# Kernel optimization log

Hardware: AMD Instinct MI355X
Metric: run time of the kernel (lower is better)

## Reference

```python
import jax, jax.numpy as jnp
import numpy as np

N_NODES = 50000


def _gcn_norm(edge_index, num_nodes):
    # Add self-loops (PyG GCNConv default) and compute symmetric norm.
    loops = jnp.arange(num_nodes, dtype=edge_index.dtype)
    src = jnp.concatenate([edge_index[0], loops])
    dst = jnp.concatenate([edge_index[1], loops])
    ones = jnp.ones(src.shape[0], dtype=jnp.float32)
    deg = jax.ops.segment_sum(ones, dst, num_segments=num_nodes)
    deg_inv_sqrt = jnp.where(deg > 0, jax.lax.rsqrt(jnp.maximum(deg, 1.0)), 0.0)
    norm = deg_inv_sqrt[src] * deg_inv_sqrt[dst]  # [E + N]
    return src, dst, norm


def _gcn_conv(x, src, dst, norm, W, b, num_nodes):
    xw = x @ W                               # [N, out]
    msg = xw[src] * norm[:, None]            # gather + scale  [E+N, out]
    out = jax.ops.segment_sum(msg, dst, num_segments=num_nodes)  # scatter-add
    return out + b


def setup_inputs() -> dict:
    key = jax.random.key(0)
    ks = jax.random.split(key, 10)
    d_in, d_h, d_out = 64, 64, 8
    n_edges = 800000
    x = jax.random.normal(ks[0], (N_NODES, d_in), dtype=jnp.float32)
    edge_index = jax.random.randint(ks[1], (2, n_edges), 0, N_NODES, dtype=jnp.int64)
    def w(k, fan_in, fan_out):
        return jax.random.normal(k, (fan_in, fan_out), dtype=jnp.float32) * (1.0 / np.sqrt(fan_in))
    return {
        "x": x,
        "edge_index": edge_index,
        "W0": w(ks[2], d_in, d_h), "b0": jnp.zeros((d_h,), jnp.float32),
        "W1": w(ks[3], d_h, d_h), "b1": jnp.zeros((d_h,), jnp.float32),
        "W2": w(ks[4], d_h, d_h), "b2": jnp.zeros((d_h,), jnp.float32),
        "linW": w(ks[5], d_h, d_out), "linb": jnp.zeros((d_out,), jnp.float32),
    }


def reference(x, edge_index, W0, b0, W1, b1, W2, b2, linW, linb):
    num_nodes = x.shape[0]
    src, dst, norm = _gcn_norm(edge_index, num_nodes)
    # 3 GCNConv layers, ReLU; dropout is identity at inference (training=False).
    for W, b in ((W0, b0), (W1, b1), (W2, b2)):
        x = jax.nn.relu(_gcn_conv(x, src, dst, norm, W, b, num_nodes))
    return x @ linW + linb
```

## Files before the change

kernel.cpp:

```cpp
#include <hip/hip_runtime.h>
#include <hip/hip_fp16.h>

#define TPB 256
#define CAP 16384
#define CAPSH 14
#define SC_BLOCKS 1024
#define MAXE 4

typedef __attribute__((ext_vector_type(8))) float f32x8;
typedef __attribute__((ext_vector_type(8))) unsigned short u16x8;


__device__ __forceinline__ int ld_idx(const void* p, long long i, int is64) {
    return is64 ? (int)((const long long*)p)[i] : ((const int*)p)[i];
}

__device__ __forceinline__ ushort4 f4_to_h4(float4 v) {
    ushort4 r;
    r.x = __half_as_ushort(__float2half_rn(v.x));
    r.y = __half_as_ushort(__float2half_rn(v.y));
    r.z = __half_as_ushort(__float2half_rn(v.z));
    r.w = __half_as_ushort(__float2half_rn(v.w));
    return r;
}

__global__ __launch_bounds__(TPB) void p3_scatter(const void* __restrict__ ei,
                                                  long long E,
                                                  int* __restrict__ gcur,
                                                  int* __restrict__ pairs) {
    __shared__ int cnt[TPB];
    __shared__ int cur2[TPB];
    __shared__ int s_is64;
    int t = threadIdx.x;
    if (t < 64) {
        const unsigned int* w = (const unsigned int*)ei;
        unsigned long long m = __ballot(w[2 * t + 1] != 0u);
        if (t == 0) s_is64 = (m == 0ull) ? 1 : 0;
    }
    cnt[t] = 0;
    __syncthreads();
    const int is64 = s_is64;
    long long chunk = (E + SC_BLOCKS - 1) / SC_BLOCKS;
    long long s0 = (long long)blockIdx.x * chunk;
    long long s1 = (s0 + chunk < E) ? s0 + chunk : E;

    int pk[MAXE];
    int bk[MAXE];
    int ne = 0;
    #pragma unroll
    for (int i = 0; i < MAXE; ++i) {
        long long e = s0 + t + (long long)i * TPB;
        if (e < s1) {
            int sv = ld_idx(ei, e, is64);
            int d  = ld_idx(ei, E + e, is64);
            pk[i] = (sv << 8) | (d & 255);
            bk[i] = d >> 8;
            atomicAdd(&cnt[bk[i]], 1);
            ne++;
        }
    }
    __syncthreads();
    if (cnt[t]) cur2[t] = (t << CAPSH) + atomicAdd(&gcur[t], cnt[t]);
    __syncthreads();
    #pragma unroll
    for (int i = 0; i < MAXE; ++i) {
        if (i < ne) {
            int pos = atomicAdd(&cur2[bk[i]], 1);
            pairs[pos] = pk[i];
        }
    }
}

__global__ __launch_bounds__(TPB) void p4_fill(const int* __restrict__ pairs,
                                               const int* __restrict__ gcur,
                                               int2* __restrict__ meta,
                                               int* __restrict__ csr, int N) {
    __shared__ int ldeg[TPB];
    __shared__ int ssc[TPB];
    __shared__ int cur[TPB];
    int t = threadIdx.x;
    int b = blockIdx.x;
    int base = b << CAPSH;
    int ecnt = gcur[b];
    ldeg[t] = 0;
    __syncthreads();
    for (int e = base + t; e < base + ecnt; e += TPB)
        atomicAdd(&ldeg[pairs[e] & 255], 1);
    __syncthreads();
    int dv = ldeg[t];
    int pv = (dv + 7) & ~7;
    ssc[t] = pv;
    __syncthreads();
    for (int off = 1; off < TPB; off <<= 1) {
        int u = 0;
        if (t >= off) u = ssc[t - off];
        __syncthreads();
        ssc[t] += u;
        __syncthreads();
    }
    int o = base + ssc[t] - pv;
    cur[t] = o;
    float dd = rsqrtf((float)(dv + 1));
    int node = (b << 8) + t;
    if (node < N)
        meta[node] = make_int2((o << 8) | (pv >> 3), __float_as_int(dd));
    __syncthreads();
    for (int e = base + t; e < base + ecnt; e += TPB) {
        int p = pairs[e];
        int pos = atomicAdd(&cur[p & 255], 1);
        csr[pos] = p >> 8;
    }
    for (int e = o + dv; e < o + pv; ++e) csr[e] = N;
}

__global__ __launch_bounds__(TPB) void p5_z0(const float* __restrict__ x,
                                             const int2* __restrict__ meta,
                                             ushort4* __restrict__ z0, int N) {
    int idx = blockIdx.x * TPB + threadIdx.x;
    int node = idx >> 4, c = idx & 15;
    if (node > N) return;
    if (node == N) {
        z0[(size_t)N * 16 + c] = make_ushort4(0, 0, 0, 0);
        return;
    }
    float dv = __int_as_float(meta[node].y);
    float4 h = ((const float4*)x)[(size_t)node * 16 + c];
    float4 r = {h.x * dv, h.y * dv, h.z * dv, h.w * dv};
    z0[(size_t)node * 16 + c] = f4_to_h4(r);
}

__device__ __forceinline__ f32x8 gather_rows(const u16x8* __restrict__ z8,
                                             const int* __restrict__ csr,
                                             int start, int nbatch, int c,
                                             f32x8 acc) {
    const int base = threadIdx.x & 56;
    int idx = (nbatch > 0) ? csr[start + c] : 0;
    for (int bt = 0; bt < nbatch; ++bt) {
        int nidx = (bt + 1 < nbatch) ? csr[start + (bt + 1) * 8 + c] : 0;
        #pragma unroll
        for (int k = 0; k < 8; ++k) {
            int s = __shfl(idx, base + k);
            u16x8 v = z8[(size_t)s * 8 + c];
            #pragma unroll
            for (int i = 0; i < 8; ++i)
                acc[i] += __half2float(__ushort_as_half(v[i]));
        }
        idx = nidx;
    }
    return acc;
}

__device__ __forceinline__ f32x8 shfl_mm8(f32x8 s, const float4* Ws4, int c) {
    const int base = threadIdx.x & 56;
    f32x8 u = {0.f, 0.f, 0.f, 0.f, 0.f, 0.f, 0.f, 0.f};
    #pragma unroll
    for (int q = 0; q < 8; ++q) {
        #pragma unroll
        for (int r = 0; r < 8; ++r) {
            float hv = __shfl(s[r], base + q);
            float4 w0 = Ws4[(q * 8 + r) * 16 + 2 * c];
            float4 w1 = Ws4[(q * 8 + r) * 16 + 2 * c + 1];
            u[0] = fmaf(hv, w0.x, u[0]);
            u[1] = fmaf(hv, w0.y, u[1]);
            u[2] = fmaf(hv, w0.z, u[2]);
            u[3] = fmaf(hv, w0.w, u[3]);
            u[4] = fmaf(hv, w1.x, u[4]);
            u[5] = fmaf(hv, w1.y, u[5]);
            u[6] = fmaf(hv, w1.z, u[6]);
            u[7] = fmaf(hv, w1.w, u[7]);
        }
    }
    return u;
}

__device__ __forceinline__ u16x8 f8_to_h8(f32x8 v) {
    u16x8 r;
    #pragma unroll
    for (int i = 0; i < 8; ++i)
        r[i] = __half_as_ushort(__float2half_rn(v[i]));
    return r;
}

__global__ __launch_bounds__(TPB) void layer_mm(const u16x8* __restrict__ z,
                                                const int* __restrict__ csr,
                                                const int2* __restrict__ meta,
                                                const float* __restrict__ b,
                                                const float* __restrict__ W,
                                                u16x8* __restrict__ zout, int n) {
    __shared__ float Ws[64 * 64];
    int t = threadIdx.x;
    float4* Ws4 = (float4*)Ws;
    const float4* W4g = (const float4*)W;
    #pragma unroll
    for (int i = 0; i < 4; ++i) Ws4[t + i * TPB] = W4g[t + i * TPB];

    if (blockIdx.x == 0 && t < 8) {
        u16x8 zz = {0, 0, 0, 0, 0, 0, 0, 0};
        zout[(size_t)n * 8 + t] = zz;
    }

    int wave = t >> 6, lane = t & 63;
    int g = lane >> 3, c = lane & 7;
    int node = blockIdx.x * 32 + wave * 8 + g;
    f32x8 s = {0.f, 0.f, 0.f, 0.f, 0.f, 0.f, 0.f, 0.f};
    float dv = 0.f;
    if (node < n) {
        int2 m = meta[node];
        int start = ((unsigned)m.x) >> 8;
        int nbatch = m.x & 255;
        dv = __int_as_float(m.y);
        u16x8 v = z[(size_t)node * 8 + c];
        #pragma unroll
        for (int i = 0; i < 8; ++i) s[i] = __half2float(__ushort_as_half(v[i]));
        s = gather_rows(z, csr, start, nbatch, c, s);
    }
    __syncthreads();
    f32x8 u = shfl_mm8(s, Ws4, c);
    if (node < n) {
        float4 b0 = ((const float4*)b)[2 * c];
        float4 b1 = ((const float4*)b)[2 * c + 1];
        f32x8 r;
        r[0] = fmaxf(fmaf(dv, u[0], b0.x), 0.f) * dv;
        r[1] = fmaxf(fmaf(dv, u[1], b0.y), 0.f) * dv;
        r[2] = fmaxf(fmaf(dv, u[2], b0.z), 0.f) * dv;
        r[3] = fmaxf(fmaf(dv, u[3], b0.w), 0.f) * dv;
        r[4] = fmaxf(fmaf(dv, u[4], b1.x), 0.f) * dv;
        r[5] = fmaxf(fmaf(dv, u[5], b1.y), 0.f) * dv;
        r[6] = fmaxf(fmaf(dv, u[6], b1.z), 0.f) * dv;
        r[7] = fmaxf(fmaf(dv, u[7], b1.w), 0.f) * dv;
        zout[(size_t)node * 8 + c] = f8_to_h8(r);
    }
}

__global__ __launch_bounds__(TPB) void layer_final(const u16x8* __restrict__ z,
                                                   const int* __restrict__ csr,
                                                   const int2* __restrict__ meta,
                                                   const float* __restrict__ b,
                                                   const float* __restrict__ W,
                                                   const float* __restrict__ Wl,
                                                   const float* __restrict__ bl,
                                                   float* __restrict__ out, int n) {
    __shared__ float Ws[64 * 64];
    __shared__ float Wls[64 * 8];
    __shared__ float bls[8];
    int t = threadIdx.x;
    float4* Ws4 = (float4*)Ws;
    const float4* W4g = (const float4*)W;
    #pragma unroll
    for (int i = 0; i < 4; ++i) Ws4[t + i * TPB] = W4g[t + i * TPB];
    if (t < 128) ((float4*)Wls)[t] = ((const float4*)Wl)[t];
    if (t < 8) bls[t] = bl[t];

    int wave = t >> 6, lane = t & 63;
    int g = lane >> 3, c = lane & 7;
    int node = blockIdx.x * 32 + wave * 8 + g;
    f32x8 s = {0.f, 0.f, 0.f, 0.f, 0.f, 0.f, 0.f, 0.f};
    float dv = 0.f;
    if (node < n) {
        int2 m = meta[node];
        int start = ((unsigned)m.x) >> 8;
        int nbatch = m.x & 255;
        dv = __int_as_float(m.y);
        u16x8 v = z[(size_t)node * 8 + c];
        #pragma unroll
        for (int i = 0; i < 8; ++i) s[i] = __half2float(__ushort_as_half(v[i]));
        s = gather_rows(z, csr, start, nbatch, c, s);
    }
    __syncthreads();
    f32x8 u = shfl_mm8(s, Ws4, c);
    float4 b0 = ((const float4*)b)[2 * c];
    float4 b1 = ((const float4*)b)[2 * c + 1];
    f32x8 h;
    h[0] = fmaxf(fmaf(dv, u[0], b0.x), 0.f);
    h[1] = fmaxf(fmaf(dv, u[1], b0.y), 0.f);
    h[2] = fmaxf(fmaf(dv, u[2], b0.z), 0.f);
    h[3] = fmaxf(fmaf(dv, u[3], b0.w), 0.f);
    h[4] = fmaxf(fmaf(dv, u[4], b1.x), 0.f);
    h[5] = fmaxf(fmaf(dv, u[5], b1.y), 0.f);
    h[6] = fmaxf(fmaf(dv, u[6], b1.z), 0.f);
    h[7] = fmaxf(fmaf(dv, u[7], b1.w), 0.f);

    const int base = threadIdx.x & 56;
    float acc = bls[c];
    #pragma unroll
    for (int q = 0; q < 8; ++q) {
        #pragma unroll
        for (int r = 0; r < 8; ++r) {
            float hv = __shfl(h[r], base + q);
            acc = fmaf(hv, Wls[(q * 8 + r) * 8 + c], acc);
        }
    }
    if (node < n) out[(size_t)node * 8 + c] = acc;
}

extern "C" void kernel_launch(void* const* d_in, const int* in_sizes, int n_in,
                              void* d_out, int out_size, void* d_ws, size_t ws_size,
                              hipStream_t stream) {
    const float* x  = (const float*)d_in[0];
    const void*  ei = d_in[1];
    const float* W0 = (const float*)d_in[2];
    const float* b0 = (const float*)d_in[3];
    const float* W1 = (const float*)d_in[4];
    const float* b1 = (const float*)d_in[5];
    const float* W2 = (const float*)d_in[6];
    const float* b2 = (const float*)d_in[7];
    const float* Wl = (const float*)d_in[8];
    const float* bl = (const float*)d_in[9];

    const long long E = in_sizes[1] / 2;
    const int dh = in_sizes[3];
    const int din = in_sizes[2] / dh;
    const int N = in_sizes[0] / din;
    const int nb = (N + 255) >> 8;

    char* ws = (char*)d_ws;
    size_t off = 0;
    auto alloc = [&](size_t bytes) -> char* {
        char* r = ws + off;
        off += (bytes + 255) & ~(size_t)255;
        return r;
    };
    int*   gcur    = (int*)  alloc(1024);
    int2*  meta    = (int2*) alloc((size_t)N * 8);
    int*   pairs   = (int*)  alloc((size_t)nb * CAP * 4);
    int*   csr     = (int*)  alloc((size_t)nb * CAP * 4);
    u16x8* zbA     = (u16x8*)alloc((size_t)(N + 1) * 64 * 2);
    u16x8* zbB     = (u16x8*)alloc((size_t)(N + 1) * 64 * 2);

    hipMemsetAsync(gcur, 0, 256 * sizeof(int), stream);
    p3_scatter<<<SC_BLOCKS, TPB, 0, stream>>>(ei, E, gcur, pairs);
    p4_fill<<<nb, TPB, 0, stream>>>(pairs, gcur, meta, csr, N);
    const int gz = ((N + 1) * 16 + TPB - 1) / TPB;
    p5_z0<<<gz, TPB, 0, stream>>>(x, meta, (ushort4*)zbA, N);

    const int gL = (N + 31) / 32;
    layer_mm<<<gL, TPB, 0, stream>>>(zbA, csr, meta, b0, W0, zbB, N);
    layer_mm<<<gL, TPB, 0, stream>>>(zbB, csr, meta, b1, W1, zbA, N);
    layer_final<<<gL, TPB, 0, stream>>>(zbA, csr, meta, b2, W2, Wl, bl,
                                        (float*)d_out, N);
}
```

Baseline: 196.8 us.

## Build CSR via global degree count, scan, and atomic fill instead of bucketed scatter

Replaces the two-pass bucket scatter (pairs buffer plus per-bucket local sort) with a classic three-pass CSR build: a global atomic degree histogram, a per-256-node block scan that writes meta and cursors, and an atomic fill that places each source directly at its final slot. This drops the intermediate pairs buffer and its extra read/write pass. In exchange it reads the edge list twice and relies on contended global atomics on per-node counters and cursors, which scatter writes randomly. The order of neighbors within a row becomes nondeterministic.

```diff
diff --git a/kernel.cpp b/kernel.cpp
--- a/kernel.cpp
+++ b/kernel.cpp
@@ -4,8 +4,7 @@
 #define TPB 256
 #define CAP 16384
 #define CAPSH 14
-#define SC_BLOCKS 1024
-#define MAXE 4
+#define EG_BLOCKS 2048
 
 typedef __attribute__((ext_vector_type(8))) float f32x8;
 typedef __attribute__((ext_vector_type(8))) unsigned short u16x8;
@@ -24,12 +23,9 @@
     return r;
 }
 
-__global__ __launch_bounds__(TPB) void p3_scatter(const void* __restrict__ ei,
-                                                  long long E,
-                                                  int* __restrict__ gcur,
-                                                  int* __restrict__ pairs) {
-    __shared__ int cnt[TPB];
-    __shared__ int cur2[TPB];
+__global__ __launch_bounds__(TPB) void p1_deg(const void* __restrict__ ei,
+                                              long long E,
+                                              int* __restrict__ deg) {
     __shared__ int s_is64;
     int t = threadIdx.x;
     if (t < 64) {
@@ -37,57 +33,24 @@
         unsigned long long m = __ballot(w[2 * t + 1] != 0u);
         if (t == 0) s_is64 = (m == 0ull) ? 1 : 0;
     }
-    cnt[t] = 0;
     __syncthreads();
     const int is64 = s_is64;
-    long long chunk = (E + SC_BLOCKS - 1) / SC_BLOCKS;
-    long long s0 = (long long)blockIdx.x * chunk;
-    long long s1 = (s0 + chunk < E) ? s0 + chunk : E;
-
-    int pk[MAXE];
-    int bk[MAXE];
-    int ne = 0;
-    #pragma unroll
-    for (int i = 0; i < MAXE; ++i) {
-        long long e = s0 + t + (long long)i * TPB;
-        if (e < s1) {
-            int sv = ld_idx(ei, e, is64);
-            int d  = ld_idx(ei, E + e, is64);
-            pk[i] = (sv << 8) | (d & 255);
-            bk[i] = d >> 8;
-            atomicAdd(&cnt[bk[i]], 1);
-            ne++;
-        }
-    }
-    __syncthreads();
-    if (cnt[t]) cur2[t] = (t << CAPSH) + atomicAdd(&gcur[t], cnt[t]);
-    __syncthreads();
-    #pragma unroll
-    for (int i = 0; i < MAXE; ++i) {
-        if (i < ne) {
-            int pos = atomicAdd(&cur2[bk[i]], 1);
-            pairs[pos] = pk[i];
-        }
-    }
-}
-
-__global__ __launch_bounds__(TPB) void p4_fill(const int* __restrict__ pairs,
-                                               const int* __restrict__ gcur,
+    long long stride = (long long)gridDim.x * TPB;
+    for (long long e = (long long)blockIdx.x * TPB + t; e < E; e += stride) {
+        int d = ld_idx(ei, E + e, is64);
+        atomicAdd(&deg[d], 1);
+    }
+}
+
+__global__ __launch_bounds__(TPB) void p2_scan(const int* __restrict__ deg,
                                                int2* __restrict__ meta,
+                                               int* __restrict__ cursor,
                                                int* __restrict__ csr, int N) {
-    __shared__ int ldeg[TPB];
     __shared__ int ssc[TPB];
-    __shared__ int cur[TPB];
     int t = threadIdx.x;
     int b = blockIdx.x;
-    int base = b << CAPSH;
-    int ecnt = gcur[b];
-    ldeg[t] = 0;
-    __syncthreads();
-    for (int e = base + t; e < base + ecnt; e += TPB)
-        atomicAdd(&ldeg[pairs[e] & 255], 1);
-    __syncthreads();
-    int dv = ldeg[t];
+    int node = (b << 8) + t;
+    int dv = (node < N) ? deg[node] : 0;
     int pv = (dv + 7) & ~7;
     ssc[t] = pv;
     __syncthreads();
@@ -98,23 +61,39 @@
         ssc[t] += u;
         __syncthreads();
     }
-    int o = base + ssc[t] - pv;
-    cur[t] = o;
-    float dd = rsqrtf((float)(dv + 1));
-    int node = (b << 8) + t;
-    if (node < N)
+    int o = (b << CAPSH) + ssc[t] - pv;
+    if (node < N) {
+        float dd = rsqrtf((float)(dv + 1));
         meta[node] = make_int2((o << 8) | (pv >> 3), __float_as_int(dd));
-    __syncthreads();
-    for (int e = base + t; e < base + ecnt; e += TPB) {
-        int p = pairs[e];
-        int pos = atomicAdd(&cur[p & 255], 1);
-        csr[pos] = p >> 8;
+        cursor[node] = o;
     }
     for (int e = o + dv; e < o + pv; ++e) csr[e] = N;
 }
 
+__global__ __launch_bounds__(TPB) void p3_fill(const void* __restrict__ ei,
+                                               long long E,
+                                               int* __restrict__ cursor,
+                                               int* __restrict__ csr) {
+    __shared__ int s_is64;
+    int t = threadIdx.x;
+    if (t < 64) {
+        const unsigned int* w = (const unsigned int*)ei;
+        unsigned long long m = __ballot(w[2 * t + 1] != 0u);
+        if (t == 0) s_is64 = (m == 0ull) ? 1 : 0;
+    }
+    __syncthreads();
+    const int is64 = s_is64;
+    long long stride = (long long)gridDim.x * TPB;
+    for (long long e = (long long)blockIdx.x * TPB + t; e < E; e += stride) {
+        int sv = ld_idx(ei, e, is64);
+        int d  = ld_idx(ei, E + e, is64);
+        int pos = atomicAdd(&cursor[d], 1);
+        csr[pos] = sv;
+    }
+}
+
 __global__ __launch_bounds__(TPB) void p5_z0(const float* __restrict__ x,
-                                             const int2* __restrict__ meta,
+                                             const int* __restrict__ deg,
                                              ushort4* __restrict__ z0, int N) {
     int idx = blockIdx.x * TPB + threadIdx.x;
     int node = idx >> 4, c = idx & 15;
@@ -123,7 +102,7 @@
         z0[(size_t)N * 16 + c] = make_ushort4(0, 0, 0, 0);
         return;
     }
-    float dv = __int_as_float(meta[node].y);
+    float dv = rsqrtf((float)(deg[node] + 1));
     float4 h = ((const float4*)x)[(size_t)node * 16 + c];
     float4 r = {h.x * dv, h.y * dv, h.z * dv, h.w * dv};
     z0[(size_t)node * 16 + c] = f4_to_h4(r);
@@ -312,6 +291,7 @@
     const int din = in_sizes[2] / dh;
     const int N = in_sizes[0] / din;
     const int nb = (N + 255) >> 8;
+    const int nn = nb << 8;
 
     char* ws = (char*)d_ws;
     size_t off = 0;
@@ -320,18 +300,19 @@
         off += (bytes + 255) & ~(size_t)255;
         return r;
     };
-    int*   gcur    = (int*)  alloc(1024);
+    int*   deg     = (int*)  alloc((size_t)nn * 4);
+    int*   cursor  = (int*)  alloc((size_t)nn * 4);
     int2*  meta    = (int2*) alloc((size_t)N * 8);
-    int*   pairs   = (int*)  alloc((size_t)nb * CAP * 4);
     int*   csr     = (int*)  alloc((size_t)nb * CAP * 4);
     u16x8* zbA     = (u16x8*)alloc((size_t)(N + 1) * 64 * 2);
     u16x8* zbB     = (u16x8*)alloc((size_t)(N + 1) * 64 * 2);
 
-    hipMemsetAsync(gcur, 0, 256 * sizeof(int), stream);
-    p3_scatter<<<SC_BLOCKS, TPB, 0, stream>>>(ei, E, gcur, pairs);
-    p4_fill<<<nb, TPB, 0, stream>>>(pairs, gcur, meta, csr, N);
+    hipMemsetAsync(deg, 0, (size_t)nn * 4, stream);
+    p1_deg<<<EG_BLOCKS, TPB, 0, stream>>>(ei, E, deg);
+    p2_scan<<<nb, TPB, 0, stream>>>(deg, meta, cursor, csr, N);
+    p3_fill<<<EG_BLOCKS, TPB, 0, stream>>>(ei, E, cursor, csr);
     const int gz = ((N + 1) * 16 + TPB - 1) / TPB;
-    p5_z0<<<gz, TPB, 0, stream>>>(x, meta, (ushort4*)zbA, N);
+    p5_z0<<<gz, TPB, 0, stream>>>(x, deg, (ushort4*)zbA, N);
 
     const int gL = (N + 31) / 32;
     layer_mm<<<gL, TPB, 0, stream>>>(zbA, csr, meta, b0, W0, zbB, N);
```

Measured after the change: 253.3 us. 28.7% more time.
